# Kernel optimization log

Measured on AMD Instinct MI355X. Metric: run time of the kernel, lower is better.

Reference implementation:

```python
import jax, jax.numpy as jnp
import numpy as np

N_NODES = 50000
N_EDGES = 800000
D_IN = 64
D_OUT = 64


def setup_inputs() -> dict:
    key = jax.random.key(0)
    k1, k2, k3, k4, k5 = jax.random.split(key, 5)
    edge_attr = jax.random.normal(k1, (N_EDGES, D_IN), dtype=jnp.float32)
    edge_index = jax.random.randint(k2, (2, N_EDGES), 0, N_NODES, dtype=jnp.int64)
    node_attr = jax.random.normal(k3, (N_NODES, D_IN), dtype=jnp.float32)
    W = jax.random.normal(k4, (D_OUT, D_IN), dtype=jnp.float32) / np.sqrt(D_IN)
    b = jax.random.normal(k5, (D_OUT,), dtype=jnp.float32) * 0.01
    return {"edge_attr": edge_attr, "edge_index": edge_index, "node_attr": node_attr, "W": W, "b": b}


def reference(edge_attr, edge_index, node_attr, W, b):
    num_nodes = node_attr.shape[0]
    src = edge_index[0]
    dst = edge_index[1]
    # scatter_mean of edge_attr onto src nodes (empty segments -> 0)
    agg_sum = jax.ops.segment_sum(edge_attr, src, num_segments=num_nodes)  # [N, d_in]
    counts = jax.ops.segment_sum(jnp.ones((edge_attr.shape[0],), dtype=edge_attr.dtype), src, num_segments=num_nodes)
    edge_agg_mean = agg_sum / jnp.clip(counts, 1.0)[:, None]
    mean_sum_embedds = node_attr + edge_agg_mean * 0.5  # [N, d_in]
    node_embeddings = jax.nn.sigmoid(mean_sum_embedds @ W.T + b)  # [N, d_out]
    edge_embeddings = (node_embeddings[src] + node_embeddings[dst]) * 0.5  # [E, d_out]
    return edge_embeddings
```

## Files before the change

kernel.cpp:

```cpp
#include <hip/hip_runtime.h>
#include <math.h>

#define N_NODES 50000
#define N_EDGES 800000
#define D 64
#define NB_SCAN ((N_NODES + 255) / 256)

typedef float f32x4 __attribute__((ext_vector_type(4)));

__global__ __launch_bounds__(256) void hist_kernel(
    const int* __restrict__ edge_index, int* __restrict__ cnt)
{
    int e = blockIdx.x * blockDim.x + threadIdx.x;
    if (e >= N_EDGES) return;
    atomicAdd(&cnt[edge_index[e]], 1);
}

__global__ __launch_bounds__(256) void scanA_kernel(
    const int* __restrict__ cnt, int* __restrict__ offs, int* __restrict__ bsum)
{
    __shared__ int tmp[256];
    int tid = threadIdx.x;
    int i = blockIdx.x * 256 + tid;
    int v = (i < N_NODES) ? cnt[i] : 0;
    tmp[tid] = v;
    __syncthreads();
    for (int s = 1; s < 256; s <<= 1) {
        int add = (tid >= s) ? tmp[tid - s] : 0;
        __syncthreads();
        tmp[tid] += add;
        __syncthreads();
    }
    if (i < N_NODES) offs[i] = tmp[tid] - v;
    if (tid == 255) bsum[blockIdx.x] = tmp[255];
}

__global__ __launch_bounds__(256) void scanB_kernel(int* __restrict__ bsum)
{
    __shared__ int tmp[256];
    int tid = threadIdx.x;
    int v = (tid < NB_SCAN) ? bsum[tid] : 0;
    tmp[tid] = v;
    __syncthreads();
    for (int s = 1; s < 256; s <<= 1) {
        int add = (tid >= s) ? tmp[tid - s] : 0;
        __syncthreads();
        tmp[tid] += add;
        __syncthreads();
    }
    bsum[tid] = tmp[tid] - v;
}

__global__ __launch_bounds__(256) void scanC_kernel(
    int* __restrict__ offs, const int* __restrict__ bsum, int* __restrict__ cursor)
{
    int i = blockIdx.x * 256 + threadIdx.x;
    if (i >= N_NODES) return;
    int o = offs[i] + bsum[blockIdx.x];
    offs[i] = o;
    cursor[i] = o;
}

__global__ __launch_bounds__(256) void fill_kernel(
    const int* __restrict__ edge_index, int* __restrict__ cursor,
    int* __restrict__ bucket)
{
    int e = blockIdx.x * blockDim.x + threadIdx.x;
    if (e >= N_EDGES) return;
    int src = edge_index[e];
    int pos = atomicAdd(&cursor[src], 1);
    bucket[pos] = e;
}

__global__ __launch_bounds__(256) void node_fused_kernel(
    const float* __restrict__ node_attr,
    const float* __restrict__ edge_attr,
    const int* __restrict__ cnt,
    const int* __restrict__ offs,
    const int* __restrict__ bucket,
    const float* __restrict__ W,
    const float* __restrict__ bias,
    float* __restrict__ node_emb)
{
    __shared__ float Wt[D * (D + 1)];
    int tid = threadIdx.x;
    for (int k = tid; k < D * D; k += 256) {
        int o = k >> 6, i = k & 63;
        Wt[i * (D + 1) + o] = W[k];
    }
    __syncthreads();

    int n = blockIdx.x * 4 + (tid >> 6);
    int lane = tid & 63;
    if (n >= N_NODES) return;

    int c   = cnt[n];
    int beg = offs[n];
    const int* __restrict__ bk = bucket + beg;

    float s0 = 0.f, s1 = 0.f, s2 = 0.f, s3 = 0.f;
    float s4 = 0.f, s5 = 0.f, s6 = 0.f, s7 = 0.f;
    int k = 0;
    for (; k + 8 <= c; k += 8) {
        int e0 = bk[k + 0], e1 = bk[k + 1], e2 = bk[k + 2], e3 = bk[k + 3];
        int e4 = bk[k + 4], e5 = bk[k + 5], e6 = bk[k + 6], e7 = bk[k + 7];
        s0 += edge_attr[(size_t)e0 * D + lane];
        s1 += edge_attr[(size_t)e1 * D + lane];
        s2 += edge_attr[(size_t)e2 * D + lane];
        s3 += edge_attr[(size_t)e3 * D + lane];
        s4 += edge_attr[(size_t)e4 * D + lane];
        s5 += edge_attr[(size_t)e5 * D + lane];
        s6 += edge_attr[(size_t)e6 * D + lane];
        s7 += edge_attr[(size_t)e7 * D + lane];
    }
    for (; k + 4 <= c; k += 4) {
        int e0 = bk[k + 0], e1 = bk[k + 1], e2 = bk[k + 2], e3 = bk[k + 3];
        s0 += edge_attr[(size_t)e0 * D + lane];
        s1 += edge_attr[(size_t)e1 * D + lane];
        s2 += edge_attr[(size_t)e2 * D + lane];
        s3 += edge_attr[(size_t)e3 * D + lane];
    }
    for (; k < c; ++k) {
        int e0 = bk[k];
        s0 += edge_attr[(size_t)e0 * D + lane];
    }
    float sum = ((s0 + s1) + (s2 + s3)) + ((s4 + s5) + (s6 + s7));

    float scale = 0.5f / (float)((c > 0) ? c : 1);
    float ms = node_attr[(size_t)n * D + lane] + sum * scale;

    float acc = bias[lane];
    #pragma unroll
    for (int i = 0; i < D; ++i) {
        acc = fmaf(__shfl(ms, i, 64), Wt[i * (D + 1) + lane], acc);
    }
    node_emb[(size_t)n * D + lane] = 1.0f / (1.0f + __expf(-acc));
}

__global__ __launch_bounds__(256) void edge_kernel(
    const int* __restrict__ edge_index,
    const f32x4* __restrict__ node_emb,
    f32x4* __restrict__ out)
{
    int t = blockIdx.x * blockDim.x + threadIdx.x;
    if (t >= N_EDGES * 16) return;
    int e = t >> 4;
    int q = t & 15;
    int src = edge_index[e];
    int dst = edge_index[N_EDGES + e];
    f32x4 a = node_emb[src * 16 + q];
    f32x4 c = node_emb[dst * 16 + q];
    f32x4 r = (a + c) * 0.5f;
    __builtin_nontemporal_store(r, out + t);
}

extern "C" void kernel_launch(void* const* d_in, const int* in_sizes, int n_in,
                              void* d_out, int out_size, void* d_ws, size_t ws_size,
                              hipStream_t stream) {
    const float* edge_attr  = (const float*)d_in[0];
    const int*   edge_index = (const int*)d_in[1];
    const float* node_attr  = (const float*)d_in[2];
    const float* W          = (const float*)d_in[3];
    const float* bias       = (const float*)d_in[4];
    float* out = (float*)d_out;

    char* ws = (char*)d_ws;
    int*   cnt      = (int*)(ws);
    int*   offs     = (int*)(ws + 200000);
    int*   bsum     = (int*)(ws + 400000);
    int*   cursor   = (int*)(ws + 401024);
    int*   bucket   = (int*)(ws + 601024);
    float* node_emb = (float*)(ws + 3801024);

    hipMemsetAsync(cnt, 0, N_NODES * sizeof(int), stream);

    hist_kernel<<<(N_EDGES + 255) / 256, 256, 0, stream>>>(edge_index, cnt);
    scanA_kernel<<<NB_SCAN, 256, 0, stream>>>(cnt, offs, bsum);
    scanB_kernel<<<1, 256, 0, stream>>>(bsum);
    scanC_kernel<<<NB_SCAN, 256, 0, stream>>>(offs, bsum, cursor);
    fill_kernel<<<(N_EDGES + 255) / 256, 256, 0, stream>>>(edge_index, cursor, bucket);
    node_fused_kernel<<<(N_NODES + 3) / 4, 256, 0, stream>>>(
        node_attr, edge_attr, cnt, offs, bucket, W, bias, node_emb);
    edge_kernel<<<(N_EDGES * 16 + 255) / 256, 256, 0, stream>>>(
        edge_index, (const f32x4*)node_emb, (f32x4*)out);
}
```

Baseline: 537.5 us.

## Vectorize edge gather with float4 per sub-wave and widen edge kernel per thread

The node kernel now splits each 64-lane wave into four 16-lane groups. Each group gathers a different edge row with 16-byte non-temporal float4 loads, and the partial sums are combined with xor shuffles. The matvec shuffle is adapted to the new per-lane float4 layout. The edge kernel now handles two float4 chunks per thread, halving the thread count and the redundant index loads. The intent is fewer, wider memory transactions and more edges in flight per wave, at the cost of extra shuffle reductions and more register use.

Measured after the change: 547.7 us. Within noise of the previous version (+1.9%).

```diff
diff --git a/kernel.cpp b/kernel.cpp
--- a/kernel.cpp
+++ b/kernel.cpp
@@ -98,41 +98,46 @@
     int beg = offs[n];
     const int* __restrict__ bk = bucket + beg;
 
-    float s0 = 0.f, s1 = 0.f, s2 = 0.f, s3 = 0.f;
-    float s4 = 0.f, s5 = 0.f, s6 = 0.f, s7 = 0.f;
+    int sub = lane >> 4;
+    int q   = lane & 15;
+
+    f32x4 s0 = {0.f,0.f,0.f,0.f}, s1 = s0, s2 = s0, s3 = s0;
     int k = 0;
-    for (; k + 8 <= c; k += 8) {
-        int e0 = bk[k + 0], e1 = bk[k + 1], e2 = bk[k + 2], e3 = bk[k + 3];
-        int e4 = bk[k + 4], e5 = bk[k + 5], e6 = bk[k + 6], e7 = bk[k + 7];
-        s0 += edge_attr[(size_t)e0 * D + lane];
-        s1 += edge_attr[(size_t)e1 * D + lane];
-        s2 += edge_attr[(size_t)e2 * D + lane];
-        s3 += edge_attr[(size_t)e3 * D + lane];
-        s4 += edge_attr[(size_t)e4 * D + lane];
-        s5 += edge_attr[(size_t)e5 * D + lane];
-        s6 += edge_attr[(size_t)e6 * D + lane];
-        s7 += edge_attr[(size_t)e7 * D + lane];
+    for (; k + 16 <= c; k += 16) {
+        int ea = bk[k +  0 + sub];
+        int eb = bk[k +  4 + sub];
+        int ec = bk[k +  8 + sub];
+        int ed = bk[k + 12 + sub];
+        s0 += __builtin_nontemporal_load((const f32x4*)(edge_attr + (size_t)ea * D) + q);
+        s1 += __builtin_nontemporal_load((const f32x4*)(edge_attr + (size_t)eb * D) + q);
+        s2 += __builtin_nontemporal_load((const f32x4*)(edge_attr + (size_t)ec * D) + q);
+        s3 += __builtin_nontemporal_load((const f32x4*)(edge_attr + (size_t)ed * D) + q);
     }
     for (; k + 4 <= c; k += 4) {
-        int e0 = bk[k + 0], e1 = bk[k + 1], e2 = bk[k + 2], e3 = bk[k + 3];
-        s0 += edge_attr[(size_t)e0 * D + lane];
-        s1 += edge_attr[(size_t)e1 * D + lane];
-        s2 += edge_attr[(size_t)e2 * D + lane];
-        s3 += edge_attr[(size_t)e3 * D + lane];
+        int ea = bk[k + sub];
+        s0 += __builtin_nontemporal_load((const f32x4*)(edge_attr + (size_t)ea * D) + q);
     }
-    for (; k < c; ++k) {
-        int e0 = bk[k];
-        s0 += edge_attr[(size_t)e0 * D + lane];
+    int rem = c - k;
+    if (sub < rem) {
+        int ea = bk[k + sub];
+        s1 += __builtin_nontemporal_load((const f32x4*)(edge_attr + (size_t)ea * D) + q);
     }
-    float sum = ((s0 + s1) + (s2 + s3)) + ((s4 + s5) + (s6 + s7));
+    f32x4 s = (s0 + s1) + (s2 + s3);
+
+    s.x += __shfl_xor(s.x, 16, 64); s.y += __shfl_xor(s.y, 16, 64);
+    s.z += __shfl_xor(s.z, 16, 64); s.w += __shfl_xor(s.w, 16, 64);
+    s.x += __shfl_xor(s.x, 32, 64); s.y += __shfl_xor(s.y, 32, 64);
+    s.z += __shfl_xor(s.z, 32, 64); s.w += __shfl_xor(s.w, 32, 64);
 
     float scale = 0.5f / (float)((c > 0) ? c : 1);
-    float ms = node_attr[(size_t)n * D + lane] + sum * scale;
+    f32x4 na = __builtin_nontemporal_load((const f32x4*)(node_attr + (size_t)n * D) + q);
+    f32x4 ms = na + s * scale;
 
     float acc = bias[lane];
     #pragma unroll
     for (int i = 0; i < D; ++i) {
-        acc = fmaf(__shfl(ms, i, 64), Wt[i * (D + 1) + lane], acc);
+        float m = __shfl(ms[i & 3], i >> 2, 64);
+        acc = fmaf(m, Wt[i * (D + 1) + lane], acc);
     }
     node_emb[(size_t)n * D + lane] = 1.0f / (1.0f + __expf(-acc));
 }
@@ -143,15 +148,17 @@
     f32x4* __restrict__ out)
 {
     int t = blockIdx.x * blockDim.x + threadIdx.x;
-    if (t >= N_EDGES * 16) return;
-    int e = t >> 4;
-    int q = t & 15;
+    if (t >= N_EDGES * 8) return;
+    int e = t >> 3;
+    int q = t & 7;
     int src = edge_index[e];
     int dst = edge_index[N_EDGES + e];
-    f32x4 a = node_emb[src * 16 + q];
-    f32x4 c = node_emb[dst * 16 + q];
-    f32x4 r = (a + c) * 0.5f;
-    __builtin_nontemporal_store(r, out + t);
+    f32x4 a0 = node_emb[src * 16 + 2 * q];
+    f32x4 a1 = node_emb[src * 16 + 2 * q + 1];
+    f32x4 c0 = node_emb[dst * 16 + 2 * q];
+    f32x4 c1 = node_emb[dst * 16 + 2 * q + 1];
+    __builtin_nontemporal_store((a0 + c0) * 0.5f, out + 2 * t);
+    __builtin_nontemporal_store((a1 + c1) * 0.5f, out + 2 * t + 1);
 }
 
 extern "C" void kernel_launch(void* const* d_in, const int* in_sizes, int n_in,
@@ -181,6 +188,6 @@
     fill_kernel<<<(N_EDGES + 255) / 256, 256, 0, stream>>>(edge_index, cursor, bucket);
     node_fused_kernel<<<(N_NODES + 3) / 4, 256, 0, stream>>>(
         node_attr, edge_attr, cnt, offs, bucket, W, bias, node_emb);
-    edge_kernel<<<(N_EDGES * 16 + 255) / 256, 256, 0, stream>>>(
+    edge_kernel<<<(N_EDGES * 8 + 255) / 256, 256, 0, stream>>>(
         edge_index, (const f32x4*)node_emb, (f32x4*)out);
 }
```
